# Kernel optimization log

Measured on AMD Instinct MI355X. Metric: run time of the kernel, lower is better.

## Reference

```python
import jax, jax.numpy as jnp
import numpy as np

N, E, B = 20000, 200000, 16
ND, ED, GD, HD, DOF = 64, 32, 32, 128, 6
PI = 3.14159265358979

def _hat(v):
    x, y, z = v[..., 0], v[..., 1], v[..., 2]
    O = jnp.zeros_like(x)
    return jnp.stack([jnp.stack([O, -z, y], -1),
                      jnp.stack([z, O, -x], -1),
                      jnp.stack([-y, x, O], -1)], -2)

def _so3_exp(phi):
    th2 = jnp.sum(phi * phi, -1, keepdims=True)
    th = jnp.sqrt(th2 + 1e-12)
    a = jnp.where(th < 1e-4, 1.0 - th2 / 6.0, jnp.sin(th) / th)
    b = jnp.where(th < 1e-4, 0.5 - th2 / 24.0, (1.0 - jnp.cos(th)) / th2)
    K = _hat(phi)
    I = jnp.eye(3, dtype=phi.dtype)
    return I + a[..., None] * K + b[..., None] * (K @ K)

def _se3_exp(rho, phi):
    # returns (R, t) of Exp([rho, phi]) with rotation part phi
    th2 = jnp.sum(phi * phi, -1, keepdims=True)
    th = jnp.sqrt(th2 + 1e-12)
    a = jnp.where(th < 1e-4, 1.0 - th2 / 6.0, jnp.sin(th) / th)
    b = jnp.where(th < 1e-4, 0.5 - th2 / 24.0, (1.0 - jnp.cos(th)) / th2)
    c = jnp.where(th < 1e-4, 1.0 / 6.0 - th2 / 120.0, (th - jnp.sin(th)) / (th2 * th))
    K = _hat(phi)
    KK = K @ K
    I = jnp.eye(3, dtype=phi.dtype)
    R = I + a[..., None] * K + b[..., None] * KK
    V = I + b[..., None] * K + c[..., None] * KK
    t = jnp.einsum('nij,nj->ni', V, rho)
    return R, t

def _comp(Ra, ta, Rb, tb):
    return Ra @ Rb, jnp.einsum('nij,nj->ni', Ra, tb) + ta

def _inv(R, t):
    Rt = jnp.swapaxes(R, -1, -2)
    return Rt, -jnp.einsum('nij,nj->ni', Rt, t)

def _vec(R, t):
    # flattened [R | t] 3x4 -> 12
    return jnp.concatenate([R, t[..., None]], -1).reshape(R.shape[0], 12)

def setup_inputs() -> dict:
    key = jax.random.key(0)
    ks = jax.random.split(key, 16)
    T_R = _so3_exp(0.5 * jax.random.normal(ks[0], (N, 3)))
    Tij_R = _so3_exp(0.5 * jax.random.normal(ks[1], (E, 3)))
    return {
        'xfeat': jax.random.normal(ks[2], (N, ND), jnp.float32),
        'T_R': T_R.astype(jnp.float32),
        'T_t': jax.random.normal(ks[3], (N, 3), jnp.float32),
        'edge_feat': jax.random.normal(ks[4], (E, ED), jnp.float32),
        'Tij_R': Tij_R.astype(jnp.float32),
        'Tij_t': jax.random.normal(ks[5], (E, 3), jnp.float32),
        'u': jax.random.normal(ks[6], (B, GD), jnp.float32),
        'edge_index': jax.random.randint(ks[7], (2, E), 0, N),
        'batch': jnp.sort(jax.random.randint(ks[8], (N,), 0, B)),
        'W1': 0.05 * jax.random.normal(ks[9], (2 * ND + 12 + ED, HD), jnp.float32),
        'b1': jnp.zeros((HD,), jnp.float32),
        'W2': 0.05 * jax.random.normal(ks[10], (HD, HD), jnp.float32),
        'b2': jnp.zeros((HD,), jnp.float32),
        'W3': 0.05 * jax.random.normal(ks[11], (HD + GD + ND, HD), jnp.float32),
        'b3': jnp.zeros((HD,), jnp.float32),
        'W4': 0.05 * jax.random.normal(ks[12], (HD, ND + DOF), jnp.float32),
        'b4': jnp.zeros((ND + DOF,), jnp.float32),
    }

def reference(xfeat, T_R, T_t, edge_feat, Tij_R, Tij_t, u,
              edge_index, batch, W1, b1, W2, b2, W3, b3, W4, b4):
    n = xfeat.shape[0]
    i, j = edge_index[0], edge_index[1]
    xfi, xfj = xfeat[i], xfeat[j]
    Ri, ti = T_R[i], T_t[i]
    Rj, tj = T_R[j], T_t[j]
    # T_err_ij = Tj * Ti.inv() * Tij_hat.inv()
    Rii, tii = _inv(Ri, ti)
    Ra, ta = _comp(Rj, tj, Rii, tii)
    Rhi, thi = _inv(Tij_R, Tij_t)
    Reij, teij = _comp(Ra, ta, Rhi, thi)
    # T_err_ji = Ti * Tj.inv() * Tij_hat
    Rji_, tji_ = _inv(Rj, tj)
    Rb, tb = _comp(Ri, ti, Rji_, tji_)
    Reji, teji = _comp(Rb, tb, Tij_R, Tij_t)
    f_ij = jnp.concatenate([xfi, xfj, edge_feat, _vec(Reij, teij)], 1)
    f_ji = jnp.concatenate([xfj, xfi, edge_feat, _vec(Reji, teji)], 1)
    feats = jnp.concatenate([f_ij, f_ji], 0)          # [2E, 172]
    j_both = jnp.concatenate([j, i], 0)               # [2E]
    h = jax.nn.relu(feats @ W1 + b1)
    h = jax.nn.relu(h @ W2 + b2)                      # [2E, HD]
    sums = jax.ops.segment_sum(h, j_both, num_segments=n)
    cnt = jax.ops.segment_sum(jnp.ones((h.shape[0], 1), h.dtype), j_both, num_segments=n)
    aggr = sums / jnp.maximum(cnt, 1.0)               # scatter_mean
    g = jnp.concatenate([aggr, xfeat, u[batch]], 1)
    out = jax.nn.relu(g @ W3 + b3) @ W4 + b4
    xupd, tupd = out[:, :-DOF], out[:, -DOF:]
    rho, phi = tupd[:, :3], tupd[:, 3:]
    # SquashRot: bound rotation angle to pi via tanh
    th = jnp.linalg.norm(phi, axis=-1, keepdims=True)
    phi = phi * (PI * jnp.tanh(th / PI) / (th + 1e-8))
    Rd, td = _se3_exp(rho, phi)
    R_out, t_out = _comp(Rd, td, T_R, T_t)            # boxplus_left: Exp(d) * T
    xfeat_out = xfeat + xupd
    theta = jnp.linalg.norm(phi, axis=-1, keepdims=True)
    return jnp.concatenate([xfeat_out, R_out.reshape(n, 9), t_out, theta], -1)
```

## Files before the change

### kernel.cpp

```cpp
#include <hip/hip_runtime.h>
#include <math.h>

#define ND 64
#define ED 32
#define GD 32
#define HD 128
#define DOF 6
#define K1 172
#define K1PAD 192
#define KG 224
#define N4P 80
#define NOUT 70
#define OUTC 77
#define MT 256
#define P1 136
#define TDN 16
#define GP 232
#define HP 136
#define OP 84
#define NMAX 20480
#define PI_F 3.14159265358979f

typedef short short8 __attribute__((ext_vector_type(8)));
typedef float f32x4  __attribute__((ext_vector_type(4)));

__device__ __forceinline__ unsigned short f2b(float f) {
    unsigned int u = __float_as_uint(f);
    u += 0x7fffu + ((u >> 16) & 1u);
    return (unsigned short)(u >> 16);
}
__device__ __forceinline__ float b2f(unsigned short b) {
    return __uint_as_float(((unsigned int)b) << 16);
}
__device__ __forceinline__ void mul33_abt(const float* A, const float* B, float* C) {
#pragma unroll
    for (int r = 0; r < 3; r++)
#pragma unroll
        for (int c = 0; c < 3; c++)
            C[3*r+c] = A[3*r+0]*B[3*c+0] + A[3*r+1]*B[3*c+1] + A[3*r+2]*B[3*c+2];
}

__global__ void __launch_bounds__(256)
prep(const float* __restrict__ W1, const float* __restrict__ W2,
     const float* __restrict__ W3, const float* __restrict__ W4,
     const float* __restrict__ xfeat, const float* __restrict__ edge_feat,
     const int* __restrict__ edge_index,
     unsigned short* __restrict__ W1b, unsigned short* __restrict__ W2b,
     unsigned short* __restrict__ W3b, unsigned short* __restrict__ W4b,
     unsigned short* __restrict__ xb, unsigned short* __restrict__ eb,
     int* __restrict__ cnti, int N, int E)
{
    int idx = blockIdx.x * 256 + threadIdx.x;
    if (idx < K1PAD * HD) {
        int k = idx >> 7, n = idx & 127;
        float v = (k < K1) ? W1[k * HD + n] : 0.f;
        int kc = k >> 5, kr = k & 31, q = kr >> 3, j = kr & 7;
        W1b[(((kc * 8 + (n >> 4)) * 4 + q) * 16 + (n & 15)) * 8 + j] = f2b(v);
        return;
    }
    idx -= K1PAD * HD;
    if (idx < HD * HD) {
        int k = idx >> 7, n = idx & 127;
        int kc = k >> 5, kr = k & 31, q = kr >> 3, j = kr & 7;
        W2b[(((kc * 8 + (n >> 4)) * 4 + q) * 16 + (n & 15)) * 8 + j] = f2b(W2[k * HD + n]);
        return;
    }
    idx -= HD * HD;
    if (idx < KG * HD) {
        int k = idx >> 7, n = idx & 127;
        int sk = (k < HD) ? ((k & 7) * 16 + (k >> 3)) : k;
        int kc = k >> 5, kr = k & 31, q = kr >> 3, j = kr & 7;
        W3b[(((kc * 8 + (n >> 4)) * 4 + q) * 16 + (n & 15)) * 8 + j] = f2b(W3[sk * HD + n]);
        return;
    }
    idx -= KG * HD;
    if (idx < HD * N4P) {
        int k = idx / N4P, n = idx % N4P;
        float v = (n < NOUT) ? W4[k * NOUT + n] : 0.f;
        int kc = k >> 5, kr = k & 31, q = kr >> 3, j = kr & 7;
        W4b[(((kc * 5 + (n >> 4)) * 4 + q) * 16 + (n & 15)) * 8 + j] = f2b(v);
        return;
    }
    idx -= HD * N4P;
    const int nx4 = N * ND / 4;
    if (idx < nx4) {
        const float4 v = *(const float4*)&xfeat[idx * 4];
        ushort4 o; o.x = f2b(v.x); o.y = f2b(v.y); o.z = f2b(v.z); o.w = f2b(v.w);
        *(ushort4*)&xb[idx * 4] = o;
        return;
    }
    idx -= nx4;
    const int ne4 = E * ED / 4;
    if (idx < ne4) {
        const float4 v = *(const float4*)&edge_feat[idx * 4];
        ushort4 o; o.x = f2b(v.x); o.y = f2b(v.y); o.z = f2b(v.z); o.w = f2b(v.w);
        *(ushort4*)&eb[idx * 4] = o;
        return;
    }
    idx -= ne4;
    if (idx < 2 * E) {
        const int tgt = (idx < E) ? edge_index[E + idx] : edge_index[idx - E];
        atomicAdd(&cnti[tgt], 1);
    }
}

__global__ void __launch_bounds__(1024)
scan_kernel(const int* __restrict__ cnti, int* __restrict__ off,
            int* __restrict__ cursor, int N)
{
    __shared__ int sh[NMAX];
    __shared__ int part[1024];
    const int t = threadIdx.x;
    for (int i = t; i < N; i += 1024) sh[i] = cnti[i];
    __syncthreads();
    const int chunk = (N + 1023) / 1024;
    const int base = t * chunk;
    int s = 0;
    for (int i = 0; i < chunk; i++) { int idx = base + i; if (idx < N) s += sh[idx]; }
    part[t] = s;
    __syncthreads();
    for (int d = 1; d < 1024; d <<= 1) {
        int v = (t >= d) ? part[t - d] : 0;
        __syncthreads();
        part[t] += v;
        __syncthreads();
    }
    int pre = (t > 0) ? part[t - 1] : 0;
    for (int i = 0; i < chunk; i++) {
        int idx = base + i;
        if (idx < N) { int c = sh[idx]; sh[idx] = pre; pre += c; }
    }
    __syncthreads();
    for (int i = t; i < N; i += 1024) { off[i] = sh[i]; cursor[i] = sh[i]; }
}

__global__ void __launch_bounds__(256)
scatter_pose(const float* __restrict__ T_R, const float* __restrict__ T_t,
             const float* __restrict__ Tij_R, const float* __restrict__ Tij_t,
             const int* __restrict__ edge_index, int* __restrict__ cursor,
             int4* __restrict__ dinfo, unsigned short* __restrict__ poseb, int E)
{
    const int g = blockIdx.x * 256 + threadIdx.x;
    if (g >= 2 * E) return;
    const bool fwd = (g < E);
    const int e = fwd ? g : g - E;
    const int ni = edge_index[e];
    const int nj = edge_index[E + e];
    const int tgt = fwd ? nj : ni;
    const int pos = atomicAdd(&cursor[tgt], 1);
    dinfo[pos] = make_int4(fwd ? ni : nj, fwd ? nj : ni, e, g);

    float Ri[9], Rj[9], TR[9], ti[3], tj[3], Tt[3];
#pragma unroll
    for (int q = 0; q < 9; q++) { Ri[q] = T_R[9*ni+q]; Rj[q] = T_R[9*nj+q]; TR[q] = Tij_R[9*e+q]; }
#pragma unroll
    for (int q = 0; q < 3; q++) { ti[q] = T_t[3*ni+q]; tj[q] = T_t[3*nj+q]; Tt[q] = Tij_t[3*e+q]; }
    float A[9];
    mul33_abt(Rj, Ri, A);
    float Re[9], te[3];
    if (fwd) {
        mul33_abt(A, TR, Re);
#pragma unroll
        for (int r = 0; r < 3; r++)
            te[r] = tj[r]
                  - (A[3*r+0]*ti[0] + A[3*r+1]*ti[1] + A[3*r+2]*ti[2])
                  - (Re[3*r+0]*Tt[0] + Re[3*r+1]*Tt[1] + Re[3*r+2]*Tt[2]);
    } else {
#pragma unroll
        for (int r = 0; r < 3; r++)
#pragma unroll
            for (int c = 0; c < 3; c++)
                Re[3*r+c] = A[r]*TR[c] + A[3+r]*TR[3+c] + A[6+r]*TR[6+c];
        const float d0 = Tt[0]-tj[0], d1 = Tt[1]-tj[1], d2 = Tt[2]-tj[2];
#pragma unroll
        for (int r = 0; r < 3; r++)
            te[r] = ti[r] + A[r]*d0 + A[3+r]*d1 + A[6+r]*d2;
    }
    short8 p0, p1;
#pragma unroll
    for (int r = 0; r < 2; r++) {
        p0[4*r+0] = (short)f2b(Re[3*r+0]);
        p0[4*r+1] = (short)f2b(Re[3*r+1]);
        p0[4*r+2] = (short)f2b(Re[3*r+2]);
        p0[4*r+3] = (short)f2b(te[r]);
    }
    p1[0] = (short)f2b(Re[6]); p1[1] = (short)f2b(Re[7]);
    p1[2] = (short)f2b(Re[8]); p1[3] = (short)f2b(te[2]);
    p1[4] = 0; p1[5] = 0; p1[6] = 0; p1[7] = 0;
    *(short8*)(poseb + (size_t)pos * 16) = p0;
    *(short8*)(poseb + (size_t)pos * 16 + 8) = p1;
}

__global__ void __launch_bounds__(256, 2)
edge_kernel(const unsigned short* __restrict__ xb, const unsigned short* __restrict__ eb,
            const unsigned short* __restrict__ poseb, const int4* __restrict__ dinfo,
            const unsigned short* __restrict__ W1b, const float* __restrict__ b1,
            const unsigned short* __restrict__ W2b, const float* __restrict__ b2,
            unsigned short* __restrict__ hbuf, int E)
{
    __shared__ unsigned short h1s[4 * 64 * P1];
    const int tid = threadIdx.x;
    const int wv = tid >> 6, lane = tid & 63;
    const int nl = lane & 15, quad = lane >> 4;
    const int D0 = blockIdx.x * MT + wv * 64;
    const int laneoff = quad * 128 + nl * 8;
    const int twoE = 2 * E;
    unsigned short* hw = h1s + wv * 64 * P1;

    int s1[4], s2[4], ee[4], pp[4];
#pragma unroll
    for (int rt = 0; rt < 4; rt++) {
        int p = D0 + rt * 16 + nl;
        if (p >= twoE) p = twoE - 1;
        pp[rt] = p;
        const int4 di = dinfo[p];
        s1[rt] = di.x; s2[rt] = di.y; ee[rt] = di.z;
    }

    f32x4 acc[4][8];
#pragma unroll
    for (int rt = 0; rt < 4; rt++)
#pragma unroll
        for (int At = 0; At < 8; At++) acc[rt][At] = (f32x4)0.f;

    short8 af[2][4], wf[2][8];
#pragma unroll
    for (int rt = 0; rt < 4; rt++)
        af[0][rt] = *(const short8*)(xb + (size_t)s1[rt] * ND + quad * 8);
#pragma unroll
    for (int nt = 0; nt < 8; nt++)
        wf[0][nt] = *(const short8*)(W1b + nt * 512 + laneoff);

#pragma unroll
    for (int kc = 0; kc < 6; kc++) {
        const int cur = kc & 1, nxt = cur ^ 1;
        if (kc < 5) {
#pragma unroll
            for (int rt = 0; rt < 4; rt++) {
                switch (kc + 1) {
                case 1: af[nxt][rt] = *(const short8*)(xb + (size_t)s1[rt] * ND + 32 + quad * 8); break;
                case 2: af[nxt][rt] = *(const short8*)(xb + (size_t)s2[rt] * ND + quad * 8); break;
                case 3: af[nxt][rt] = *(const short8*)(xb + (size_t)s2[rt] * ND + 32 + quad * 8); break;
                case 4: af[nxt][rt] = *(const short8*)(eb + (size_t)ee[rt] * ED + quad * 8); break;
                default: af[nxt][rt] = (quad < 2) ? *(const short8*)(poseb + (size_t)pp[rt] * 16 + quad * 8)
                                                  : (short8)(short)0; break;
                }
            }
#pragma unroll
            for (int nt = 0; nt < 8; nt++)
                wf[nxt][nt] = *(const short8*)(W1b + ((kc + 1) * 8 + nt) * 512 + laneoff);
        }
#pragma unroll
        for (int At = 0; At < 8; At++)
#pragma unroll
            for (int rt = 0; rt < 4; rt++)
                acc[rt][At] = __builtin_amdgcn_mfma_f32_16x16x32_bf16(wf[cur][At], af[cur][rt], acc[rt][At], 0, 0, 0);
    }

#pragma unroll
    for (int At = 0; At < 8; At++) {
        const f32x4 bv = *(const f32x4*)&b1[At * 16 + quad * 4];
#pragma unroll
        for (int rt = 0; rt < 4; rt++) {
            unsigned int lo = (unsigned int)f2b(fmaxf(acc[rt][At][0] + bv[0], 0.f))
                            | ((unsigned int)f2b(fmaxf(acc[rt][At][1] + bv[1], 0.f)) << 16);
            unsigned int hi = (unsigned int)f2b(fmaxf(acc[rt][At][2] + bv[2], 0.f))
                            | ((unsigned int)f2b(fmaxf(acc[rt][At][3] + bv[3], 0.f)) << 16);
            uint2 pk; pk.x = lo; pk.y = hi;
            *(uint2*)&hw[(rt * 16 + nl) * P1 + At * 16 + quad * 4] = pk;
        }
    }
    asm volatile("s_waitcnt lgkmcnt(0)" ::: "memory");

#pragma unroll
    for (int rt = 0; rt < 4; rt++)
#pragma unroll
        for (int nt = 0; nt < 8; nt++) acc[rt][nt] = (f32x4)0.f;
#pragma unroll
    for (int nt = 0; nt < 8; nt++)
        wf[0][nt] = *(const short8*)(W2b + nt * 512 + laneoff);
#pragma unroll
    for (int kc = 0; kc < 4; kc++) {
        short8 hf[4];
#pragma unroll
        for (int rt = 0; rt < 4; rt++)
            hf[rt] = *(const short8*)&hw[(rt * 16 + nl) * P1 + kc * 32 + quad * 8];
        const int cur = kc & 1, nxt = cur ^ 1;
        if (kc < 3) {
#pragma unroll
            for (int nt = 0; nt < 8; nt++)
                wf[nxt][nt] = *(const short8*)(W2b + ((kc + 1) * 8 + nt) * 512 + laneoff);
        }
#pragma unroll
        for (int nt = 0; nt < 8; nt++)
#pragma unroll
            for (int rt = 0; rt < 4; rt++)
                acc[rt][nt] = __builtin_amdgcn_mfma_f32_16x16x32_bf16(hf[rt], wf[cur][nt], acc[rt][nt], 0, 0, 0);
    }

    {
        float bias2[8];
#pragma unroll
        for (int nt = 0; nt < 8; nt++) bias2[nt] = b2[nt * 16 + nl];
#pragma unroll
        for (int rt = 0; rt < 4; rt++)
#pragma unroll
            for (int r = 0; r < 4; r++) {
                const int p2 = D0 + rt * 16 + quad * 4 + r;
                if (p2 < twoE) {
                    short8 hv;
#pragma unroll
                    for (int nt = 0; nt < 8; nt++)
                        hv[nt] = (short)f2b(fmaxf(acc[rt][nt][r] + bias2[nt], 0.f));
                    *(short8*)(hbuf + (size_t)p2 * HD + nl * 8) = hv;
                }
            }
    }
}

__global__ void __launch_bounds__(256)
node_kernel(const float* __restrict__ xfeat, const float* __restrict__ T_R,
            const float* __restrict__ T_t, const float* __restrict__ u,
            const int* __restrict__ batch,
            const unsigned short* __restrict__ W3b, const float* __restrict__ b3,
            const unsigned short* __restrict__ W4b, const float* __restrict__ b4,
            const unsigned short* __restrict__ hbuf, const int* __restrict__ off,
            const int* __restrict__ cnti,
            float* __restrict__ out, int Nn)
{
    __shared__ unsigned short gbuf[TDN * GP];
    __shared__ unsigned short hid[TDN * HP];
    __shared__ float obuf[TDN * OP];
    const int tid = threadIdx.x;
    const int wv = tid >> 6, lane = tid & 63;
    const int n0 = blockIdx.x * TDN;
    const int nn = min(TDN, Nn - n0);

#pragma unroll
    for (int i = 0; i < 4; i++) {
        const int d = wv + 4 * i;
        if (d < nn) {
            const int n = n0 + d;
            const int deg = cnti[n];
            const int start = off[n];
            const float inv = 1.0f / (float)max(deg, 1);
            const unsigned short* hp = hbuf + (size_t)start * HD + 2 * lane;
            float a0 = 0.f, a1 = 0.f;
            int k = 0;
            for (; k + 4 <= deg; k += 4) {
                const unsigned int v0 = *(const unsigned int*)(hp);
                const unsigned int v1 = *(const unsigned int*)(hp + HD);
                const unsigned int v2 = *(const unsigned int*)(hp + 2 * HD);
                const unsigned int v3 = *(const unsigned int*)(hp + 3 * HD);
                hp += 4 * HD;
                a0 += b2f((unsigned short)v0) + b2f((unsigned short)v1)
                    + b2f((unsigned short)v2) + b2f((unsigned short)v3);
                a1 += b2f((unsigned short)(v0 >> 16)) + b2f((unsigned short)(v1 >> 16))
                    + b2f((unsigned short)(v2 >> 16)) + b2f((unsigned short)(v3 >> 16));
            }
            for (; k < deg; k++) {
                const unsigned int v0 = *(const unsigned int*)(hp);
                hp += HD;
                a0 += b2f((unsigned short)v0);
                a1 += b2f((unsigned short)(v0 >> 16));
            }
            const unsigned int pk = (unsigned int)f2b(a0 * inv) | ((unsigned int)f2b(a1 * inv) << 16);
            *(unsigned int*)&gbuf[d * GP + 2 * lane] = pk;
        }
    }
    for (int idx = tid; idx < TDN * 24; idx += 256) {
        const int d = idx / 24;
        if (d < nn) {
            const int n = n0 + d;
            const int c4 = (idx % 24) * 4;
            float4 v;
            if (c4 < 64) v = *(const float4*)&xfeat[(size_t)n * ND + c4];
            else         v = *(const float4*)&u[(size_t)batch[n] * GD + (c4 - 64)];
            ushort4 o; o.x = f2b(v.x); o.y = f2b(v.y); o.z = f2b(v.z); o.w = f2b(v.w);
            *(ushort4*)&gbuf[d * GP + 128 + c4] = o;
        }
    }
    __syncthreads();

    const int nl = lane & 15, quad = lane >> 4;
    const int laneoff = quad * 128 + nl * 8;

    f32x4 acc3[2];
    acc3[0] = (f32x4)0.f; acc3[1] = (f32x4)0.f;
#pragma unroll
    for (int kc = 0; kc < 7; kc++) {
        short8 A0 = *(const short8*)&gbuf[nl * GP + kc * 32 + quad * 8];
#pragma unroll
        for (int t = 0; t < 2; t++) {
            short8 B = *(const short8*)(W3b + (kc * 8 + wv * 2 + t) * 512 + laneoff);
            acc3[t] = __builtin_amdgcn_mfma_f32_16x16x32_bf16(A0, B, acc3[t], 0, 0, 0);
        }
    }
#pragma unroll
    for (int t = 0; t < 2; t++) {
        const int col = (wv * 2 + t) * 16 + nl;
        const float bb = b3[col];
#pragma unroll
        for (int r = 0; r < 4; r++)
            hid[(quad * 4 + r) * HP + col] = f2b(fmaxf(acc3[t][r] + bb, 0.f));
    }
    __syncthreads();

    f32x4 acc4[2];
    acc4[0] = (f32x4)0.f; acc4[1] = (f32x4)0.f;
    const int nt1 = (wv == 0) ? 4 : -1;
#pragma unroll
    for (int kc = 0; kc < 4; kc++) {
        short8 A0 = *(const short8*)&hid[nl * HP + kc * 32 + quad * 8];
        short8 B0 = *(const short8*)(W4b + (kc * 5 + wv) * 512 + laneoff);
        acc4[0] = __builtin_amdgcn_mfma_f32_16x16x32_bf16(A0, B0, acc4[0], 0, 0, 0);
        if (nt1 >= 0) {
            short8 B1 = *(const short8*)(W4b + (kc * 5 + nt1) * 512 + laneoff);
            acc4[1] = __builtin_amdgcn_mfma_f32_16x16x32_bf16(A0, B1, acc4[1], 0, 0, 0);
        }
    }
    {
        const int col0 = wv * 16 + nl;
        const float bb0 = (col0 < NOUT) ? b4[col0] : 0.f;
#pragma unroll
        for (int r = 0; r < 4; r++)
            obuf[(quad * 4 + r) * OP + col0] = acc4[0][r] + bb0;
        if (nt1 >= 0) {
            const int col1 = nt1 * 16 + nl;
            const float bb1 = (col1 < NOUT) ? b4[col1] : 0.f;
#pragma unroll
            for (int r = 0; r < 4; r++)
                obuf[(quad * 4 + r) * OP + col1] = acc4[1][r] + bb1;
        }
    }
    __syncthreads();

    for (int idx = tid; idx < TDN * ND; idx += 256) {
        const int d = idx >> 6, c = idx & 63;
        if (d < nn) {
            const int n = n0 + d;
            out[(size_t)n * OUTC + c] = xfeat[(size_t)n * ND + c] + obuf[d * OP + c];
        }
    }
    if (tid < nn) {
        const int n = n0 + tid;
        const float r0 = obuf[tid*OP + 64], r1 = obuf[tid*OP + 65], r2 = obuf[tid*OP + 66];
        float p0 = obuf[tid*OP + 67], p1 = obuf[tid*OP + 68], p2 = obuf[tid*OP + 69];
        const float th0 = sqrtf(p0*p0 + p1*p1 + p2*p2);
        const float s = PI_F * tanhf(th0 / PI_F) / (th0 + 1e-8f);
        p0 *= s; p1 *= s; p2 *= s;
        const float pp = p0*p0 + p1*p1 + p2*p2;
        const float th = sqrtf(pp + 1e-12f);
        float a, b, c;
        if (th < 1e-4f) { a = 1.f - pp/6.f; b = 0.5f - pp/24.f; c = 1.f/6.f - pp/120.f; }
        else { const float sn = sinf(th), cs = cosf(th); a = sn/th; b = (1.f-cs)/pp; c = (th-sn)/(pp*th); }
        float Rd[9], V[9];
        Rd[0]=1.f+b*(p0*p0-pp); Rd[1]=-a*p2+b*p0*p1; Rd[2]= a*p1+b*p0*p2;
        Rd[3]= a*p2+b*p1*p0;    Rd[4]=1.f+b*(p1*p1-pp); Rd[5]=-a*p0+b*p1*p2;
        Rd[6]=-a*p1+b*p2*p0;    Rd[7]= a*p0+b*p2*p1;  Rd[8]=1.f+b*(p2*p2-pp);
        V[0]=1.f+c*(p0*p0-pp);  V[1]=-b*p2+c*p0*p1;   V[2]= b*p1+c*p0*p2;
        V[3]= b*p2+c*p1*p0;     V[4]=1.f+c*(p1*p1-pp); V[5]=-b*p0+c*p1*p2;
        V[6]=-b*p1+c*p2*p0;     V[7]= b*p0+c*p2*p1;   V[8]=1.f+c*(p2*p2-pp);
        const float td0 = V[0]*r0 + V[1]*r1 + V[2]*r2;
        const float td1 = V[3]*r0 + V[4]*r1 + V[5]*r2;
        const float td2 = V[6]*r0 + V[7]*r1 + V[8]*r2;
        float TRn[9], Ttn[3];
#pragma unroll
        for (int q = 0; q < 9; q++) TRn[q] = T_R[9*n+q];
#pragma unroll
        for (int q = 0; q < 3; q++) Ttn[q] = T_t[3*n+q];
        float* o = out + (size_t)n * OUTC + 64;
#pragma unroll
        for (int r = 0; r < 3; r++)
#pragma unroll
            for (int cc = 0; cc < 3; cc++)
                o[3*r+cc] = Rd[3*r+0]*TRn[cc] + Rd[3*r+1]*TRn[3+cc] + Rd[3*r+2]*TRn[6+cc];
        o[9]  = Rd[0]*Ttn[0] + Rd[1]*Ttn[1] + Rd[2]*Ttn[2] + td0;
        o[10] = Rd[3]*Ttn[0] + Rd[4]*Ttn[1] + Rd[5]*Ttn[2] + td1;
        o[11] = Rd[6]*Ttn[0] + Rd[7]*Ttn[1] + Rd[8]*Ttn[2] + td2;
        o[12] = sqrtf(pp);
    }
}

extern "C" void kernel_launch(void* const* d_in, const int* in_sizes, int n_in,
                              void* d_out, int out_size, void* d_ws, size_t ws_size,
                              hipStream_t stream)
{
    const float* xfeat     = (const float*)d_in[0];
    const float* T_R       = (const float*)d_in[1];
    const float* T_t       = (const float*)d_in[2];
    const float* edge_feat = (const float*)d_in[3];
    const float* Tij_R     = (const float*)d_in[4];
    const float* Tij_t     = (const float*)d_in[5];
    const float* u         = (const float*)d_in[6];
    const int*   edge_index= (const int*)d_in[7];
    const int*   batch     = (const int*)d_in[8];
    const float* W1 = (const float*)d_in[9],  *b1 = (const float*)d_in[10];
    const float* W2 = (const float*)d_in[11], *b2 = (const float*)d_in[12];
    const float* W3 = (const float*)d_in[13], *b3 = (const float*)d_in[14];
    const float* W4 = (const float*)d_in[15], *b4 = (const float*)d_in[16];
    const int N = in_sizes[0] / ND;
    const int E = in_sizes[3] / ED;

    char* p = (char*)d_ws;
    unsigned short* W1b = (unsigned short*)p;   p += (size_t)K1PAD * HD * 2;
    unsigned short* W2b = (unsigned short*)p;   p += (size_t)HD * HD * 2;
    unsigned short* W3b = (unsigned short*)p;   p += (size_t)KG * HD * 2;
    unsigned short* W4b = (unsigned short*)p;   p += (size_t)HD * N4P * 2;
    unsigned short* xb  = (unsigned short*)p;   p += (size_t)N * ND * 2;
    unsigned short* ebf = (unsigned short*)p;   p += (size_t)E * ED * 2;
    unsigned short* poseb = (unsigned short*)p; p += (size_t)2 * E * 16 * 2;
    unsigned short* hbuf = (unsigned short*)p;  p += (size_t)2 * E * HD * 2;
    int4* dinfo = (int4*)p;                     p += (size_t)2 * E * 16;
    int* cnti = (int*)p;                        p += (size_t)N * 4;
    int* off  = (int*)p;                        p += (size_t)N * 4;
    int* cursor = (int*)p;

    hipMemsetAsync(cnti, 0, (size_t)N * 4, stream);
    const int prepn = K1PAD*HD + HD*HD + KG*HD + HD*N4P + N*ND/4 + E*ED/4 + 2*E;
    prep<<<(prepn + 255) / 256, 256, 0, stream>>>(W1, W2, W3, W4, xfeat, edge_feat,
                                                  edge_index, W1b, W2b, W3b, W4b,
                                                  xb, ebf, cnti, N, E);
    scan_kernel<<<1, 1024, 0, stream>>>(cnti, off, cursor, N);
    scatter_pose<<<(2*E + 255) / 256, 256, 0, stream>>>(T_R, T_t, Tij_R, Tij_t,
                                                        edge_index, cursor, dinfo, poseb, E);
    const int ebk = (2 * E + MT - 1) / MT;
    edge_kernel<<<ebk, 256, 0, stream>>>(xb, ebf, poseb, dinfo,
                                         W1b, b1, W2b, b2, hbuf, E);
    const int nb = (N + TDN - 1) / TDN;
    node_kernel<<<nb, 256, 0, stream>>>(xfeat, T_R, T_t, u, batch, W3b, b3, W4b, b4,
                                        hbuf, off, cnti, (float*)d_out, N);
}
```

Before: 266.0 us.

## Fuse segment-sum into edge kernel via LDS accumulation and replace single-block scan

The edge kernel no longer writes a 2E x 128 bf16 hidden buffer for the node kernel to re-read and reduce. It now reduces each dst-sorted tile into a per-block LDS node accumulator and writes node sums to a float buffer. Nodes that lie entirely inside a block are stored directly, boundary nodes use global atomics, and blocks spanning too many nodes fall back to global atomics. The single-workgroup scan is replaced by a three-kernel multi-block scan. This removes a large intermediate round-trip through memory, but adds a memset of the sums buffer, atomics and extra launches.

```diff
diff --git a/kernel.cpp b/kernel.cpp
--- a/kernel.cpp
+++ b/kernel.cpp
@@ -13,12 +13,14 @@
 #define NOUT 70
 #define OUTC 77
 #define MT 256
-#define P1 136
+#define P1 132
+#define NACCP 132
+#define NACC_CAP 124
 #define TDN 16
 #define GP 232
 #define HP 136
 #define OP 84
-#define NMAX 20480
+#define SCB 2048
 #define PI_F 3.14159265358979f
 
 typedef short short8 __attribute__((ext_vector_type(8)));
@@ -68,9 +70,8 @@
     idx -= HD * HD;
     if (idx < KG * HD) {
         int k = idx >> 7, n = idx & 127;
-        int sk = (k < HD) ? ((k & 7) * 16 + (k >> 3)) : k;
         int kc = k >> 5, kr = k & 31, q = kr >> 3, j = kr & 7;
-        W3b[(((kc * 8 + (n >> 4)) * 4 + q) * 16 + (n & 15)) * 8 + j] = f2b(W3[sk * HD + n]);
+        W3b[(((kc * 8 + (n >> 4)) * 4 + q) * 16 + (n & 15)) * 8 + j] = f2b(W3[k * HD + n]);
         return;
     }
     idx -= KG * HD;
@@ -104,41 +105,52 @@
     }
 }
 
-__global__ void __launch_bounds__(1024)
-scan_kernel(const int* __restrict__ cnti, int* __restrict__ off,
-            int* __restrict__ cursor, int N)
-{
-    __shared__ int sh[NMAX];
-    __shared__ int part[1024];
+__global__ void __launch_bounds__(256)
+scan1(const int* __restrict__ cnti, int* __restrict__ off, int* __restrict__ btot, int N)
+{
+    __shared__ int sh[SCB];
+    __shared__ int tsum[256];
     const int t = threadIdx.x;
-    for (int i = t; i < N; i += 1024) sh[i] = cnti[i];
-    __syncthreads();
-    const int chunk = (N + 1023) / 1024;
-    const int base = t * chunk;
-    int s = 0;
-    for (int i = 0; i < chunk; i++) { int idx = base + i; if (idx < N) s += sh[idx]; }
-    part[t] = s;
-    __syncthreads();
-    for (int d = 1; d < 1024; d <<= 1) {
-        int v = (t >= d) ? part[t - d] : 0;
+    const int base = blockIdx.x * SCB;
+    for (int i = t; i < SCB; i += 256) { int g = base + i; sh[i] = (g < N) ? cnti[g] : 0; }
+    __syncthreads();
+    int loc[8], s = 0;
+#pragma unroll
+    for (int k = 0; k < 8; k++) { loc[k] = s; s += sh[t * 8 + k]; }
+    tsum[t] = s;
+    __syncthreads();
+    for (int d = 1; d < 256; d <<= 1) {
+        int v = (t >= d) ? tsum[t - d] : 0;
         __syncthreads();
-        part[t] += v;
+        tsum[t] += v;
         __syncthreads();
     }
-    int pre = (t > 0) ? part[t - 1] : 0;
-    for (int i = 0; i < chunk; i++) {
-        int idx = base + i;
-        if (idx < N) { int c = sh[idx]; sh[idx] = pre; pre += c; }
-    }
-    __syncthreads();
-    for (int i = t; i < N; i += 1024) { off[i] = sh[i]; cursor[i] = sh[i]; }
+    const int pre = (t > 0) ? tsum[t - 1] : 0;
+#pragma unroll
+    for (int k = 0; k < 8; k++) { int g = base + t * 8 + k; if (g < N) off[g] = pre + loc[k]; }
+    if (t == 255) btot[blockIdx.x] = tsum[255];
+}
+__global__ void __launch_bounds__(64)
+scan2(int* __restrict__ btot, int nb)
+{
+    if (threadIdx.x == 0) {
+        int s = 0;
+        for (int b = 0; b < nb; b++) { int c = btot[b]; btot[b] = s; s += c; }
+    }
+}
+__global__ void __launch_bounds__(256)
+scan3(int* __restrict__ off, const int* __restrict__ btot, int* __restrict__ cursor, int N)
+{
+    int i = blockIdx.x * 256 + threadIdx.x;
+    if (i < N) { int v = off[i] + btot[i / SCB]; off[i] = v; cursor[i] = v; }
 }
 
 __global__ void __launch_bounds__(256)
 scatter_pose(const float* __restrict__ T_R, const float* __restrict__ T_t,
              const float* __restrict__ Tij_R, const float* __restrict__ Tij_t,
              const int* __restrict__ edge_index, int* __restrict__ cursor,
-             int4* __restrict__ dinfo, unsigned short* __restrict__ poseb, int E)
+             int4* __restrict__ dinfo, int* __restrict__ p2n,
+             unsigned short* __restrict__ poseb, int E)
 {
     const int g = blockIdx.x * 256 + threadIdx.x;
     if (g >= 2 * E) return;
@@ -148,7 +160,8 @@
     const int nj = edge_index[E + e];
     const int tgt = fwd ? nj : ni;
     const int pos = atomicAdd(&cursor[tgt], 1);
-    dinfo[pos] = make_int4(fwd ? ni : nj, fwd ? nj : ni, e, g);
+    dinfo[pos] = make_int4(fwd ? ni : nj, fwd ? nj : ni, e, tgt);
+    p2n[pos] = tgt;
 
     float Ri[9], Rj[9], TR[9], ti[3], tj[3], Tt[3];
 #pragma unroll
@@ -194,18 +207,29 @@
 __global__ void __launch_bounds__(256, 2)
 edge_kernel(const unsigned short* __restrict__ xb, const unsigned short* __restrict__ eb,
             const unsigned short* __restrict__ poseb, const int4* __restrict__ dinfo,
+            const int* __restrict__ p2n, const int* __restrict__ off,
+            const int* __restrict__ cnti,
             const unsigned short* __restrict__ W1b, const float* __restrict__ b1,
             const unsigned short* __restrict__ W2b, const float* __restrict__ b2,
-            unsigned short* __restrict__ hbuf, int E)
-{
-    __shared__ unsigned short h1s[4 * 64 * P1];
+            float* __restrict__ sums, int E)
+{
+    __shared__ __align__(16) char smem[4 * 64 * P1 * 2];
+    __shared__ int sinfo[2];
+    unsigned short* h1s = (unsigned short*)smem;
+    float* nacc = (float*)smem;
     const int tid = threadIdx.x;
     const int wv = tid >> 6, lane = tid & 63;
     const int nl = lane & 15, quad = lane >> 4;
-    const int D0 = blockIdx.x * MT + wv * 64;
+    const int D0blk = blockIdx.x * MT;
+    const int D0 = D0blk + wv * 64;
     const int laneoff = quad * 128 + nl * 8;
     const int twoE = 2 * E;
     unsigned short* hw = h1s + wv * 64 * P1;
+
+    if (tid == 0) {
+        sinfo[0] = p2n[D0blk];
+        sinfo[1] = p2n[min(D0blk + MT - 1, twoE - 1)];
+    }
 
     int s1[4], s2[4], ee[4], pp[4];
 #pragma unroll
@@ -281,10 +305,13 @@
         wf[0][nt] = *(const short8*)(W2b + nt * 512 + laneoff);
 #pragma unroll
     for (int kc = 0; kc < 4; kc++) {
-        short8 hf[4];
-#pragma unroll
-        for (int rt = 0; rt < 4; rt++)
-            hf[rt] = *(const short8*)&hw[(rt * 16 + nl) * P1 + kc * 32 + quad * 8];
+        union { short8 s; uint2 u[2]; } hf[4];
+#pragma unroll
+        for (int rt = 0; rt < 4; rt++) {
+            const unsigned short* hp = &hw[(rt * 16 + nl) * P1 + kc * 32 + quad * 8];
+            hf[rt].u[0] = *(const uint2*)hp;
+            hf[rt].u[1] = *(const uint2*)(hp + 4);
+        }
         const int cur = kc & 1, nxt = cur ^ 1;
         if (kc < 3) {
 #pragma unroll
@@ -295,26 +322,67 @@
         for (int nt = 0; nt < 8; nt++)
 #pragma unroll
             for (int rt = 0; rt < 4; rt++)
-                acc[rt][nt] = __builtin_amdgcn_mfma_f32_16x16x32_bf16(hf[rt], wf[cur][nt], acc[rt][nt], 0, 0, 0);
-    }
+                acc[rt][nt] = __builtin_amdgcn_mfma_f32_16x16x32_bf16(hf[rt].s, wf[cur][nt], acc[rt][nt], 0, 0, 0);
+    }
+
+    __syncthreads();
+    const int n_first = sinfo[0];
+    const int nspan = sinfo[1] - n_first + 1;
+    const bool fb = (nspan > NACC_CAP);
+    if (!fb)
+        for (int i = tid; i < nspan * NACCP; i += 256) nacc[i] = 0.f;
+    __syncthreads();
 
     {
         float bias2[8];
 #pragma unroll
         for (int nt = 0; nt < 8; nt++) bias2[nt] = b2[nt * 16 + nl];
 #pragma unroll
-        for (int rt = 0; rt < 4; rt++)
-#pragma unroll
-            for (int r = 0; r < 4; r++) {
-                const int p2 = D0 + rt * 16 + quad * 4 + r;
-                if (p2 < twoE) {
-                    short8 hv;
-#pragma unroll
-                    for (int nt = 0; nt < 8; nt++)
-                        hv[nt] = (short)f2b(fmaxf(acc[rt][nt][r] + bias2[nt], 0.f));
-                    *(short8*)(hbuf + (size_t)p2 * HD + nl * 8) = hv;
+        for (int rt = 0; rt < 4; rt++) {
+            const int p2b = D0 + rt * 16 + quad * 4;
+            if (p2b >= twoE) continue;
+            const int4 nd = *(const int4*)(p2n + p2b);
+            const int nvals = min(4, twoE - p2b);
+            if (nvals == 4 && nd.x == nd.w) {
+                const int row = nd.x - n_first;
+#pragma unroll
+                for (int nt = 0; nt < 8; nt++) {
+                    const f32x4 a = acc[rt][nt];
+                    const float bb = bias2[nt];
+                    const float v = fmaxf(a[0] + bb, 0.f) + fmaxf(a[1] + bb, 0.f)
+                                  + fmaxf(a[2] + bb, 0.f) + fmaxf(a[3] + bb, 0.f);
+                    if (fb) unsafeAtomicAdd(&sums[(size_t)nd.x * HD + nt * 16 + nl], v);
+                    else    atomicAdd(&nacc[row * NACCP + nt * 16 + nl], v);
+                }
+            } else {
+                const int nda[4] = {nd.x, nd.y, nd.z, nd.w};
+                for (int r = 0; r < nvals; r++) {
+                    const int node = nda[r];
+                    const int row = node - n_first;
+#pragma unroll
+                    for (int nt = 0; nt < 8; nt++) {
+                        const float v = fmaxf(acc[rt][nt][r] + bias2[nt], 0.f);
+                        if (fb) unsafeAtomicAdd(&sums[(size_t)node * HD + nt * 16 + nl], v);
+                        else    atomicAdd(&nacc[row * NACCP + nt * 16 + nl], v);
+                    }
                 }
             }
+        }
+    }
+    __syncthreads();
+
+    if (!fb) {
+        for (int idx = tid; idx < nspan * HD; idx += 256) {
+            const int l = idx >> 7, col = idx & 127;
+            const int n = n_first + l;
+            const float v = nacc[l * NACCP + col];
+            const int st = off[n];
+            const int en = st + cnti[n];
+            if (st >= D0blk && en <= D0blk + MT)
+                sums[(size_t)n * HD + col] = v;
+            else
+                unsafeAtomicAdd(&sums[(size_t)n * HD + col], v);
+        }
     }
 }
 
@@ -324,8 +392,7 @@
             const int* __restrict__ batch,
             const unsigned short* __restrict__ W3b, const float* __restrict__ b3,
             const unsigned short* __restrict__ W4b, const float* __restrict__ b4,
-            const unsigned short* __restrict__ hbuf, const int* __restrict__ off,
-            const int* __restrict__ cnti,
+            const float* __restrict__ sums, const int* __restrict__ cnti,
             float* __restrict__ out, int Nn)
 {
     __shared__ unsigned short gbuf[TDN * GP];
@@ -336,36 +403,14 @@
     const int n0 = blockIdx.x * TDN;
     const int nn = min(TDN, Nn - n0);
 
-#pragma unroll
-    for (int i = 0; i < 4; i++) {
-        const int d = wv + 4 * i;
+    for (int idx = tid; idx < TDN * 64; idx += 256) {
+        const int d = idx >> 6, c2 = idx & 63;
         if (d < nn) {
             const int n = n0 + d;
-            const int deg = cnti[n];
-            const int start = off[n];
-            const float inv = 1.0f / (float)max(deg, 1);
-            const unsigned short* hp = hbuf + (size_t)start * HD + 2 * lane;
-            float a0 = 0.f, a1 = 0.f;
-            int k = 0;
-            for (; k + 4 <= deg; k += 4) {
-                const unsigned int v0 = *(const unsigned int*)(hp);
-                const unsigned int v1 = *(const unsigned int*)(hp + HD);
-                const unsigned int v2 = *(const unsigned int*)(hp + 2 * HD);
-                const unsigned int v3 = *(const unsigned int*)(hp + 3 * HD);
-                hp += 4 * HD;
-                a0 += b2f((unsigned short)v0) + b2f((unsigned short)v1)
-                    + b2f((unsigned short)v2) + b2f((unsigned short)v3);
-                a1 += b2f((unsigned short)(v0 >> 16)) + b2f((unsigned short)(v1 >> 16))
-                    + b2f((unsigned short)(v2 >> 16)) + b2f((unsigned short)(v3 >> 16));
-            }
-            for (; k < deg; k++) {
-                const unsigned int v0 = *(const unsigned int*)(hp);
-                hp += HD;
-                a0 += b2f((unsigned short)v0);
-                a1 += b2f((unsigned short)(v0 >> 16));
-            }
-            const unsigned int pk = (unsigned int)f2b(a0 * inv) | ((unsigned int)f2b(a1 * inv) << 16);
-            *(unsigned int*)&gbuf[d * GP + 2 * lane] = pk;
+            const float2 v = *(const float2*)&sums[(size_t)n * HD + 2 * c2];
+            const float inv = 1.0f / (float)max(cnti[n], 1);
+            const unsigned int pk = (unsigned int)f2b(v.x * inv) | ((unsigned int)f2b(v.y * inv) << 16);
+            *(unsigned int*)&gbuf[d * GP + 2 * c2] = pk;
         }
     }
     for (int idx = tid; idx < TDN * 24; idx += 256) {
@@ -510,24 +555,30 @@
     unsigned short* xb  = (unsigned short*)p;   p += (size_t)N * ND * 2;
     unsigned short* ebf = (unsigned short*)p;   p += (size_t)E * ED * 2;
     unsigned short* poseb = (unsigned short*)p; p += (size_t)2 * E * 16 * 2;
-    unsigned short* hbuf = (unsigned short*)p;  p += (size_t)2 * E * HD * 2;
     int4* dinfo = (int4*)p;                     p += (size_t)2 * E * 16;
+    int* p2n = (int*)p;                         p += ((size_t)2 * E + 8) * 4;
+    float* sums = (float*)p;                    p += (size_t)N * HD * 4;
     int* cnti = (int*)p;                        p += (size_t)N * 4;
     int* off  = (int*)p;                        p += (size_t)N * 4;
-    int* cursor = (int*)p;
+    int* cursor = (int*)p;                      p += (size_t)N * 4;
+    int* btot = (int*)p;
 
     hipMemsetAsync(cnti, 0, (size_t)N * 4, stream);
+    hipMemsetAsync(sums, 0, (size_t)N * HD * 4, stream);
     const int prepn = K1PAD*HD + HD*HD + KG*HD + HD*N4P + N*ND/4 + E*ED/4 + 2*E;
     prep<<<(prepn + 255) / 256, 256, 0, stream>>>(W1, W2, W3, W4, xfeat, edge_feat,
                                                   edge_index, W1b, W2b, W3b, W4b,
                                                   xb, ebf, cnti, N, E);
-    scan_kernel<<<1, 1024, 0, stream>>>(cnti, off, cursor, N);
+    const int nsb = (N + SCB - 1) / SCB;
+    scan1<<<nsb, 256, 0, stream>>>(cnti, off, btot, N);
+    scan2<<<1, 64, 0, stream>>>(btot, nsb);
+    scan3<<<(N + 255) / 256, 256, 0, stream>>>(off, btot, cursor, N);
     scatter_pose<<<(2*E + 255) / 256, 256, 0, stream>>>(T_R, T_t, Tij_R, Tij_t,
-                                                        edge_index, cursor, dinfo, poseb, E);
+                                                        edge_index, cursor, dinfo, p2n, poseb, E);
     const int ebk = (2 * E + MT - 1) / MT;
-    edge_kernel<<<ebk, 256, 0, stream>>>(xb, ebf, poseb, dinfo,
-                                         W1b, b1, W2b, b2, hbuf, E);
+    edge_kernel<<<ebk, 256, 0, stream>>>(xb, ebf, poseb, dinfo, p2n, off, cnti,
+                                         W1b, b1, W2b, b2, sums, E);
     const int nb = (N + TDN - 1) / TDN;
     node_kernel<<<nb, 256, 0, stream>>>(xfeat, T_R, T_t, u, batch, W3b, b3, W4b, b4,
-                                        hbuf, off, cnti, (float*)d_out, N);
-}
+                                        sums, cnti, (float*)d_out, N);
+}
```

After: 326.7 us. 1.23x slower.

## Split single-block scan into multi-block scan and repad hidden LDS tile

Applied to the files above, without the earlier changes.

Replaces the single 1024-thread block prefix scan over node counts with a three-kernel scan. Block-local scans over chunks of 2048 run in parallel, a tiny serial pass handles the block totals, and a fix-up pass adds them back. Separately, the LDS row pitch of the hidden tile in the edge kernel changes from 136 to 132, with fragment reads split into two 8-byte loads to keep alignment, aiming to cut bank conflicts. The scan change adds two extra kernel launches, which may offset the parallelism gained on a small array.

```diff
diff --git a/kernel.cpp b/kernel.cpp
--- a/kernel.cpp
+++ b/kernel.cpp
@@ -13,12 +13,12 @@
 #define NOUT 70
 #define OUTC 77
 #define MT 256
-#define P1 136
+#define P1 132
 #define TDN 16
 #define GP 232
 #define HP 136
 #define OP 84
-#define NMAX 20480
+#define SCB 2048
 #define PI_F 3.14159265358979f
 
 typedef short short8 __attribute__((ext_vector_type(8)));
@@ -104,34 +104,44 @@
     }
 }
 
-__global__ void __launch_bounds__(1024)
-scan_kernel(const int* __restrict__ cnti, int* __restrict__ off,
-            int* __restrict__ cursor, int N)
-{
-    __shared__ int sh[NMAX];
-    __shared__ int part[1024];
+__global__ void __launch_bounds__(256)
+scan1(const int* __restrict__ cnti, int* __restrict__ off, int* __restrict__ btot, int N)
+{
+    __shared__ int sh[SCB];
+    __shared__ int tsum[256];
     const int t = threadIdx.x;
-    for (int i = t; i < N; i += 1024) sh[i] = cnti[i];
+    const int base = blockIdx.x * SCB;
+    for (int i = t; i < SCB; i += 256) { int g = base + i; sh[i] = (g < N) ? cnti[g] : 0; }
     __syncthreads();
-    const int chunk = (N + 1023) / 1024;
-    const int base = t * chunk;
-    int s = 0;
-    for (int i = 0; i < chunk; i++) { int idx = base + i; if (idx < N) s += sh[idx]; }
-    part[t] = s;
+    int loc[8], s = 0;
+#pragma unroll
+    for (int k = 0; k < 8; k++) { loc[k] = s; s += sh[t * 8 + k]; }
+    tsum[t] = s;
     __syncthreads();
-    for (int d = 1; d < 1024; d <<= 1) {
-        int v = (t >= d) ? part[t - d] : 0;
+    for (int d = 1; d < 256; d <<= 1) {
+        int v = (t >= d) ? tsum[t - d] : 0;
         __syncthreads();
-        part[t] += v;
+        tsum[t] += v;
         __syncthreads();
     }
-    int pre = (t > 0) ? part[t - 1] : 0;
-    for (int i = 0; i < chunk; i++) {
-        int idx = base + i;
-        if (idx < N) { int c = sh[idx]; sh[idx] = pre; pre += c; }
-    }
-    __syncthreads();
-    for (int i = t; i < N; i += 1024) { off[i] = sh[i]; cursor[i] = sh[i]; }
+    const int pre = (t > 0) ? tsum[t - 1] : 0;
+#pragma unroll
+    for (int k = 0; k < 8; k++) { int g = base + t * 8 + k; if (g < N) off[g] = pre + loc[k]; }
+    if (t == 255) btot[blockIdx.x] = tsum[255];
+}
+__global__ void __launch_bounds__(64)
+scan2(int* __restrict__ btot, int nb)
+{
+    if (threadIdx.x == 0) {
+        int s = 0;
+        for (int b = 0; b < nb; b++) { int c = btot[b]; btot[b] = s; s += c; }
+    }
+}
+__global__ void __launch_bounds__(256)
+scan3(int* __restrict__ off, const int* __restrict__ btot, int* __restrict__ cursor, int N)
+{
+    int i = blockIdx.x * 256 + threadIdx.x;
+    if (i < N) { int v = off[i] + btot[i / SCB]; off[i] = v; cursor[i] = v; }
 }
 
 __global__ void __launch_bounds__(256)
@@ -281,10 +291,13 @@
         wf[0][nt] = *(const short8*)(W2b + nt * 512 + laneoff);
 #pragma unroll
     for (int kc = 0; kc < 4; kc++) {
-        short8 hf[4];
-#pragma unroll
-        for (int rt = 0; rt < 4; rt++)
-            hf[rt] = *(const short8*)&hw[(rt * 16 + nl) * P1 + kc * 32 + quad * 8];
+        union { short8 s; uint2 u[2]; } hf[4];
+#pragma unroll
+        for (int rt = 0; rt < 4; rt++) {
+            const unsigned short* hp = &hw[(rt * 16 + nl) * P1 + kc * 32 + quad * 8];
+            hf[rt].u[0] = *(const uint2*)hp;
+            hf[rt].u[1] = *(const uint2*)(hp + 4);
+        }
         const int cur = kc & 1, nxt = cur ^ 1;
         if (kc < 3) {
 #pragma unroll
@@ -295,7 +308,7 @@
         for (int nt = 0; nt < 8; nt++)
 #pragma unroll
             for (int rt = 0; rt < 4; rt++)
-                acc[rt][nt] = __builtin_amdgcn_mfma_f32_16x16x32_bf16(hf[rt], wf[cur][nt], acc[rt][nt], 0, 0, 0);
+                acc[rt][nt] = __builtin_amdgcn_mfma_f32_16x16x32_bf16(hf[rt].s, wf[cur][nt], acc[rt][nt], 0, 0, 0);
     }
 
     {
@@ -514,14 +527,18 @@
     int4* dinfo = (int4*)p;                     p += (size_t)2 * E * 16;
     int* cnti = (int*)p;                        p += (size_t)N * 4;
     int* off  = (int*)p;                        p += (size_t)N * 4;
-    int* cursor = (int*)p;
+    int* cursor = (int*)p;                      p += (size_t)N * 4;
+    int* btot = (int*)p;
 
     hipMemsetAsync(cnti, 0, (size_t)N * 4, stream);
     const int prepn = K1PAD*HD + HD*HD + KG*HD + HD*N4P + N*ND/4 + E*ED/4 + 2*E;
     prep<<<(prepn + 255) / 256, 256, 0, stream>>>(W1, W2, W3, W4, xfeat, edge_feat,
                                                   edge_index, W1b, W2b, W3b, W4b,
                                                   xb, ebf, cnti, N, E);
-    scan_kernel<<<1, 1024, 0, stream>>>(cnti, off, cursor, N);
+    const int nsb = (N + SCB - 1) / SCB;
+    scan1<<<nsb, 256, 0, stream>>>(cnti, off, btot, N);
+    scan2<<<1, 64, 0, stream>>>(btot, nsb);
+    scan3<<<(N + 255) / 256, 256, 0, stream>>>(off, btot, cursor, N);
     scatter_pose<<<(2*E + 255) / 256, 256, 0, stream>>>(T_R, T_t, Tij_R, Tij_t,
                                                         edge_index, cursor, dinfo, poseb, E);
     const int ebk = (2 * E + MT - 1) / MT;
```

New measurement: 265.6 us. No clear change (-0.1%).
